# Performance work log

Hardware: AMD Instinct MI355X
Metric: run time of the kernel (lower is better)

## Reference

```python
import jax, jax.numpy as jnp
import numpy as np
import math

B, T, D = 2, 2048, 1024
H, DH = 16, 64  # n_heads, d_head
ROPE_THETA = 10000.0


def _rope_cos_sin(seq_len, d_head, dtype):
    # inv_freq over even indices, freqs[i,j] = t_i * inv_freq_j, shape [T, d_head//2]
    inv_freq = 1.0 / (ROPE_THETA ** (jnp.arange(0, d_head, 2, dtype=jnp.float32) / d_head))
    freqs = jnp.arange(seq_len, dtype=jnp.float32)[:, None] * inv_freq[None, :]
    # emb = cat(freqs, freqs); we only ever index cos[..., :d_head//2], so keep the half
    cos = jnp.cos(freqs).astype(dtype)[None, :, None, :]  # [1,T,1,DH/2]
    sin = jnp.sin(freqs).astype(dtype)[None, :, None, :]
    return cos, sin


def _apply_rotation(x, cos, sin):
    # x: [B,T,H,DH]; rotate-half style as in the torch module
    x1, x2 = x[..., : x.shape[-1] // 2], x[..., x.shape[-1] // 2 :]
    return jnp.concatenate([x1 * cos - x2 * sin, x1 * sin + x2 * cos], axis=-1)


def setup_inputs() -> dict:
    key = jax.random.key(0)
    k1, k2, k3 = jax.random.split(key, 3)
    x = jax.random.normal(k1, (B, T, D), dtype=jnp.float32)
    # torch Linear weights stored transposed here as [in, out]; init_std=0.02
    Wqkv = jax.random.normal(k2, (D, 3 * D), dtype=jnp.float32) * 0.02
    Wout = jax.random.normal(k3, (D, D), dtype=jnp.float32) * 0.02
    return {"x": x, "Wqkv": Wqkv, "Wout": Wout}


def reference(x, Wqkv, Wout):
    b, t, d = x.shape
    qkv = x @ Wqkv  # [B,T,3D]
    q, k, v = jnp.split(qkv, 3, axis=-1)
    q = q.reshape(b, t, H, DH)
    k = k.reshape(b, t, H, DH)
    v = v.reshape(b, t, H, DH)

    cos, sin = _rope_cos_sin(t, DH, x.dtype)
    q = _apply_rotation(q, cos, sin)
    k = _apply_rotation(k, cos, sin)

    scale = 1.0 / math.sqrt(DH)
    # scores: [B,H,Tq,Tk]
    scores = jnp.einsum("bqhd,bkhd->bhqk", q, k) * scale
    causal = jnp.triu(jnp.ones((t, t), dtype=bool), k=1)
    scores = jnp.where(causal[None, None, :, :], -jnp.inf, scores)
    attn = jax.nn.softmax(scores, axis=-1)
    # dropout in eval mode -> identity
    out = jnp.einsum("bhqk,bkhd->bqhd", attn, v).reshape(b, t, d)
    return out @ Wout
```

## Files before the change

kernel.cpp:

```cpp
#include <hip/hip_runtime.h>
#include <hip/hip_bf16.h>
#include <stdint.h>
#include <math.h>

#define T_SEQ 2048
#define NHEAD 16
#define NBH   32
#define BTROW 4096

typedef __bf16 bf16_t;
typedef __bf16 bf16x4_t __attribute__((ext_vector_type(4)));
typedef __bf16 bf16x8_t __attribute__((ext_vector_type(8)));
typedef float  f32x4_t  __attribute__((ext_vector_type(4)));

#define QSCALE 0.18033688011112042f

__device__ __forceinline__ f32x4_t mfma16(bf16x8_t a, bf16x8_t b, f32x4_t c) {
  return __builtin_amdgcn_mfma_f32_16x16x32_bf16(a, b, c, 0, 0, 0);
}

__device__ __forceinline__ float fast_exp2(float x) {
#if __has_builtin(__builtin_amdgcn_exp2f)
  return __builtin_amdgcn_exp2f(x);
#else
  return exp2f(x);
#endif
}

__device__ __forceinline__ void gl_lds16(const bf16_t* g, bf16_t* l) {
  __builtin_amdgcn_global_load_lds(
      (const __attribute__((address_space(1))) void*)g,
      (__attribute__((address_space(3))) void*)l, 16, 0, 0);
}

__global__ __launch_bounds__(256) void k_cast_bf16(const float* __restrict__ in,
                                                   bf16_t* __restrict__ out, int n) {
  int tid = blockIdx.x * blockDim.x + threadIdx.x;
  int stride = gridDim.x * blockDim.x;
  for (int i = tid * 4; i < n; i += stride * 4) {
    float4 a = *(const float4*)(in + i);
    bf16x4_t r = { (bf16_t)a.x, (bf16_t)a.y, (bf16_t)a.z, (bf16_t)a.w };
    *(bf16x4_t*)(out + i) = r;
  }
}

__global__ __launch_bounds__(256) void k_trans_cast(const float* __restrict__ W,
                                                    bf16_t* __restrict__ WT,
                                                    int K, int N) {
  __shared__ float tile[32][33];
  int n0 = blockIdx.x * 32, k0 = blockIdx.y * 32;
  int tx = threadIdx.x & 31, ty = threadIdx.x >> 5;
#pragma unroll
  for (int j = 0; j < 4; j++)
    tile[ty + j * 8][tx] = W[(size_t)(k0 + ty + j * 8) * N + n0 + tx];
  __syncthreads();
#pragma unroll
  for (int j = 0; j < 4; j++)
    WT[(size_t)(n0 + ty + j * 8) * K + k0 + tx] = (bf16_t)tile[tx][ty + j * 8];
}

__global__ __launch_bounds__(256) void k_rope_table(float* __restrict__ cs,
                                                    float* __restrict__ sn) {
  int i = blockIdx.x * blockDim.x + threadIdx.x;
  if (i >= T_SEQ * 32) return;
  int t = i >> 5, j = i & 31;
  float inv = powf(10000.0f, -(float)(2 * j) / 64.0f);
  float f = (float)t * inv;
  cs[i] = cosf(f);
  sn[i] = sinf(f);
}

__global__ __launch_bounds__(256) void k_gemm_qkv(const bf16_t* __restrict__ A,
                                                  const bf16_t* __restrict__ Bt,
                                                  const float* __restrict__ cs,
                                                  const float* __restrict__ sn,
                                                  bf16_t* __restrict__ Qr,
                                                  bf16_t* __restrict__ Kr,
                                                  bf16_t* __restrict__ Vt) {
  const int K = 1024;
  __shared__ __align__(16) unsigned char smem[128 * 132 * 2];
  bf16_t* As = (bf16_t*)smem;
  bf16_t* Bs = (bf16_t*)(smem + 8192);
  bf16_t* vtile = (bf16_t*)smem;

  int m0 = blockIdx.y * 128, n0 = blockIdx.x * 128;
  int tid = threadIdx.x;
  int lane = tid & 63, w = tid >> 6;
  int wr = w >> 1, wc = w & 1;
  int l15 = lane & 15, l4 = lane >> 4;

  f32x4_t acc[4][4];
#pragma unroll
  for (int m = 0; m < 4; m++)
#pragma unroll
    for (int n = 0; n < 4; n++) acc[m][n] = (f32x4_t){0.f, 0.f, 0.f, 0.f};

  for (int k0 = 0; k0 < K; k0 += 32) {
#pragma unroll
    for (int j = 0; j < 2; j++) {
      int c = j * 256 + tid;
      int row = c >> 2, kb = c & 3;
      gl_lds16(A + (size_t)(m0 + row) * K + k0 + kb * 8, As + (size_t)(j * 256 + w * 64) * 8);
      gl_lds16(Bt + (size_t)(n0 + row) * K + k0 + kb * 8, Bs + (size_t)(j * 256 + w * 64) * 8);
    }
    __syncthreads();
    bf16x8_t af[4], bfr[4];
#pragma unroll
    for (int m = 0; m < 4; m++)
      af[m] = *(const bf16x8_t*)(As + (size_t)(wr * 64 + m * 16 + l15) * 32 + l4 * 8);
#pragma unroll
    for (int n = 0; n < 4; n++)
      bfr[n] = *(const bf16x8_t*)(Bs + (size_t)(wc * 64 + n * 16 + l15) * 32 + l4 * 8);
#pragma unroll
    for (int m = 0; m < 4; m++)
#pragma unroll
      for (int n = 0; n < 4; n++) acc[m][n] = mfma16(af[m], bfr[n], acc[m][n]);
    __syncthreads();
  }

  int region = n0 >> 10;
  if (region < 2) {
    bf16_t* dst = region ? Kr : Qr;
    float qs = region ? 1.0f : QSCALE;
    int h = ((n0 & 1023) + wc * 64) >> 6;
#pragma unroll
    for (int m = 0; m < 4; m++)
#pragma unroll
      for (int r = 0; r < 4; r++) {
        int row = m0 + wr * 64 + m * 16 + l4 * 4 + r;
        int b = row >> 11, t = row & 2047;
        size_t obase = ((size_t)(b * NHEAD + h) * T_SEQ + t) * 64;
#pragma unroll
        for (int n = 0; n < 2; n++) {
          int j = n * 16 + l15;
          float c = cs[t * 32 + j], s = sn[t * 32 + j];
          float x1 = acc[m][n][r], x2 = acc[m][n + 2][r];
          dst[obase + j]      = (bf16_t)((x1 * c - x2 * s) * qs);
          dst[obase + 32 + j] = (bf16_t)((x1 * s + x2 * c) * qs);
        }
      }
  } else {
#pragma unroll
    for (int m = 0; m < 4; m++)
#pragma unroll
      for (int n = 0; n < 4; n++)
#pragma unroll
        for (int r = 0; r < 4; r++)
          vtile[(size_t)(wc * 64 + n * 16 + l15) * 132 + wr * 64 + m * 16 + l4 * 4 + r] =
              (bf16_t)acc[m][n][r];
    __syncthreads();
    int colbase = n0 - 2048;
    int b = m0 >> 11, t0l = m0 & 2047;
#pragma unroll
    for (int p = 0; p < 64; p++) {
      int idx = p * 256 + tid;
      int dl = idx >> 7, tl = idx & 127;
      int col = colbase + dl, h = col >> 6, d = col & 63;
      Vt[((size_t)(b * NHEAD + h) * 64 + d) * T_SEQ + t0l + tl] = vtile[(size_t)dl * 132 + tl];
    }
  }
}

__global__ __launch_bounds__(256) void k_gemm2(const bf16_t* __restrict__ A,
                                               const bf16_t* __restrict__ Bt,
                                               float* __restrict__ C) {
  const int N = 1024, K = 1024;
  __shared__ __align__(16) bf16_t As[64 * 32];
  __shared__ __align__(16) bf16_t Bs[128 * 32];
  int m0 = blockIdx.y * 64, n0 = blockIdx.x * 128;
  int tid = threadIdx.x;
  int lane = tid & 63, w = tid >> 6;
  int l15 = lane & 15, l4 = lane >> 4;

  f32x4_t acc[4][2];
#pragma unroll
  for (int m = 0; m < 4; m++)
#pragma unroll
    for (int n = 0; n < 2; n++) acc[m][n] = (f32x4_t){0.f, 0.f, 0.f, 0.f};

  for (int k0 = 0; k0 < K; k0 += 32) {
    {
      int row = tid >> 2, kb = tid & 3;
      gl_lds16(A + (size_t)(m0 + row) * K + k0 + kb * 8, As + (size_t)(w * 64) * 8);
    }
#pragma unroll
    for (int j = 0; j < 2; j++) {
      int c = j * 256 + tid;
      int row = c >> 2, kb = c & 3;
      gl_lds16(Bt + (size_t)(n0 + row) * K + k0 + kb * 8, Bs + (size_t)(j * 256 + w * 64) * 8);
    }
    __syncthreads();
    bf16x8_t af[4], bfr[2];
#pragma unroll
    for (int m = 0; m < 4; m++)
      af[m] = *(const bf16x8_t*)(As + (size_t)(m * 16 + l15) * 32 + l4 * 8);
#pragma unroll
    for (int n = 0; n < 2; n++)
      bfr[n] = *(const bf16x8_t*)(Bs + (size_t)(w * 32 + n * 16 + l15) * 32 + l4 * 8);
#pragma unroll
    for (int m = 0; m < 4; m++)
#pragma unroll
      for (int n = 0; n < 2; n++) acc[m][n] = mfma16(af[m], bfr[n], acc[m][n]);
    __syncthreads();
  }
#pragma unroll
  for (int m = 0; m < 4; m++)
#pragma unroll
    for (int n = 0; n < 2; n++)
#pragma unroll
      for (int r = 0; r < 4; r++) {
        int row = m0 + m * 16 + l4 * 4 + r;
        int col = n0 + w * 32 + n * 16 + l15;
        C[(size_t)row * N + col] = acc[m][n][r];
      }
}

__global__ __launch_bounds__(512, 4) void k_attn(const bf16_t* __restrict__ Qr,
                                                 const bf16_t* __restrict__ Kr,
                                                 const bf16_t* __restrict__ Vt,
                                                 bf16_t* __restrict__ Ob) {
  __shared__ __align__(16) bf16_t Ks[2][64 * 64];
  __shared__ __align__(16) bf16_t Vs[2][64 * 64];
  __shared__ __align__(16) bf16_t Ps[128 * 72];
  int flat = blockIdx.x;
  int swz = (flat & 7) * 64 + (flat >> 3);
  int pidx = swz & 15, bh = swz >> 4;
  int b = bh >> 4, h = bh & 15;
  int tid = threadIdx.x, lane = tid & 63, w = tid >> 6;
  int grp = w >> 2, wl = w & 3;
  int l15 = lane & 15, l4 = lane >> 4;

  int qb = grp ? (31 - pidx) : pidx;
  int nit = qb + 1;
  int nit_max = 32 - pidx;
  int q0 = qb * 64;

  const bf16_t* Kbh = Kr + (size_t)bh * T_SEQ * 64;
  const bf16_t* Vbh = Vt + (size_t)bh * 64 * T_SEQ;

  int srow = tid >> 3;
  int sk8 = (tid & 7) ^ (srow & 7);

  auto stage = [&](int buf, int it) {
    int kb = it * 64;
    gl_lds16(Kbh + (size_t)(kb + srow) * 64 + sk8 * 8, Ks[buf] + (size_t)(w * 64) * 8);
    gl_lds16(Vbh + (size_t)srow * T_SEQ + kb + sk8 * 8, Vs[buf] + (size_t)(w * 64) * 8);
  };

  bf16x8_t qf[2];
  size_t qbase = ((size_t)bh * T_SEQ + q0 + wl * 16 + l15) * 64;
  qf[0] = *(const bf16x8_t*)(Qr + qbase + l4 * 8);
  qf[1] = *(const bf16x8_t*)(Qr + qbase + 32 + l4 * 8);

  bf16x8_t ones;
#pragma unroll
  for (int i = 0; i < 8; i++) ones[i] = (bf16_t)1.0f;

  f32x4_t o[4];
#pragma unroll
  for (int n = 0; n < 4; n++) o[n] = (f32x4_t){0.f, 0.f, 0.f, 0.f};
  f32x4_t ls = (f32x4_t){0.f, 0.f, 0.f, 0.f};
  float m_s = -1e30f;

  stage(0, 0);

  for (int it = 0; it < nit_max; it++) {
    int cur = it & 1;
    asm volatile("s_waitcnt vmcnt(0)" ::: "memory");
    __builtin_amdgcn_s_barrier();
    if (it + 1 < nit_max) stage(cur ^ 1, it + 1);

    if (it < nit) {
      f32x4_t s[4];
      __builtin_amdgcn_s_setprio(1);
#pragma unroll
      for (int n = 0; n < 4; n++) {
        int rowK = n * 16 + l15;
        const bf16_t* kp = Ks[cur] + (size_t)rowK * 64;
        int sw = rowK & 7;
        bf16x8_t kf0 = *(const bf16x8_t*)(kp + (l4 ^ sw) * 8);
        bf16x8_t kf1 = *(const bf16x8_t*)(kp + ((l4 ^ 4) ^ sw) * 8);
        s[n] = (f32x4_t){0.f, 0.f, 0.f, 0.f};
        s[n] = mfma16(kf0, qf[0], s[n]);
        s[n] = mfma16(kf1, qf[1], s[n]);
      }
      __builtin_amdgcn_s_setprio(0);

      if (it == qb) {
#pragma unroll
        for (int n = 0; n < 4; n++)
#pragma unroll
          for (int r = 0; r < 4; r++)
            if (n * 16 + l4 * 4 + r > wl * 16 + l15) s[n][r] = -1e30f;
      }

      float t0 = fmaxf(fmaxf(s[0][0], s[0][1]), fmaxf(s[0][2], s[0][3]));
      float t1 = fmaxf(fmaxf(s[1][0], s[1][1]), fmaxf(s[1][2], s[1][3]));
      float t2 = fmaxf(fmaxf(s[2][0], s[2][1]), fmaxf(s[2][2], s[2][3]));
      float t3 = fmaxf(fmaxf(s[3][0], s[3][1]), fmaxf(s[3][2], s[3][3]));
      float mx = fmaxf(fmaxf(t0, t1), fmaxf(t2, t3));
      mx = fmaxf(mx, __shfl_xor(mx, 16, 64));
      mx = fmaxf(mx, __shfl_xor(mx, 32, 64));

      if (__any(mx - m_s > 8.0f)) {
        float mnew = fmaxf(m_s, mx);
        float alpha = fast_exp2(m_s - mnew);
        m_s = mnew;
        float ar[4];
#pragma unroll
        for (int r = 0; r < 4; r++) ar[r] = __shfl(alpha, l4 * 4 + r, 64);
#pragma unroll
        for (int n = 0; n < 4; n++)
#pragma unroll
          for (int r = 0; r < 4; r++) o[n][r] *= ar[r];
#pragma unroll
        for (int r = 0; r < 4; r++) ls[r] *= ar[r];
      }

#pragma unroll
      for (int n = 0; n < 4; n++) {
#pragma unroll
        for (int r = 0; r < 4; r++) s[n][r] = fast_exp2(s[n][r] - m_s);
        bf16x4_t pk = { (bf16_t)s[n][0], (bf16_t)s[n][1], (bf16_t)s[n][2], (bf16_t)s[n][3] };
        *(bf16x4_t*)(Ps + (size_t)(w * 16 + l15) * 72 + n * 16 + l4 * 4) = pk;
      }

      __builtin_amdgcn_s_setprio(1);
#pragma unroll
      for (int ks = 0; ks < 2; ks++) {
        bf16x8_t pa = *(const bf16x8_t*)(Ps + (size_t)(w * 16 + l15) * 72 + ks * 32 + l4 * 8);
        ls = mfma16(pa, ones, ls);
#pragma unroll
        for (int n = 0; n < 4; n++) {
          int rowV = n * 16 + l15;
          bf16x8_t vf = *(const bf16x8_t*)(Vs[cur] + (size_t)rowV * 64 +
                                           (((ks * 4 + l4) ^ (rowV & 7)) * 8));
          o[n] = mfma16(pa, vf, o[n]);
        }
      }
      __builtin_amdgcn_s_setprio(0);
    }
  }

#pragma unroll
  for (int r = 0; r < 4; r++) {
    float ir = 1.0f / ls[r];
    int q = q0 + wl * 16 + l4 * 4 + r;
    size_t off = ((size_t)(b * T_SEQ + q)) * 1024 + h * 64;
#pragma unroll
    for (int n = 0; n < 4; n++)
      Ob[off + n * 16 + l15] = (bf16_t)(o[n][r] * ir);
  }
}

extern "C" void kernel_launch(void* const* d_in, const int* in_sizes, int n_in,
                              void* d_out, int out_size, void* d_ws, size_t ws_size,
                              hipStream_t stream) {
  const float* x    = (const float*)d_in[0];
  const float* Wqkv = (const float*)d_in[1];
  const float* Wout = (const float*)d_in[2];
  float* out = (float*)d_out;
  char* ws = (char*)d_ws;

  bf16_t* wqkvT = (bf16_t*)(ws + 0);
  bf16_t* woutT = (bf16_t*)(ws + 6291456);
  bf16_t* xb    = (bf16_t*)(ws + 8388608);
  bf16_t* Qr    = (bf16_t*)(ws + 41943040);
  bf16_t* Kr    = (bf16_t*)(ws + 50331648);
  bf16_t* Vt    = (bf16_t*)(ws + 58720256);
  float*  cs    = (float*)(ws + 67108864);
  float*  sn    = (float*)(ws + 67371008);
  bf16_t* Ob    = xb;

  k_cast_bf16<<<2048, 256, 0, stream>>>(x, xb, 4096 * 1024);
  k_trans_cast<<<dim3(3072 / 32, 1024 / 32), 256, 0, stream>>>(Wqkv, wqkvT, 1024, 3072);
  k_trans_cast<<<dim3(1024 / 32, 1024 / 32), 256, 0, stream>>>(Wout, woutT, 1024, 1024);
  k_rope_table<<<(T_SEQ * 32) / 256, 256, 0, stream>>>(cs, sn);

  k_gemm_qkv<<<dim3(3072 / 128, 4096 / 128), 256, 0, stream>>>(xb, wqkvT, cs, sn, Qr, Kr, Vt);
  k_attn<<<512, 512, 0, stream>>>(Qr, Kr, Vt, Ob);
  k_gemm2<<<dim3(1024 / 128, 4096 / 64), 256, 0, stream>>>(Ob, woutT, out);
}
```

Measured before the change: 116.6 us.

## Double-buffer GEMM K-loops and split attention KV tiles across wave groups

Both GEMM kernels now double-buffer their LDS tiles so the next K-slice is prefetched while the current one runs through MFMA, with one barrier per step instead of two. The attention kernel is restructured: each block handles its paired Q tiles in two sequential passes. Within each pass the two wave groups split the KV tiles between them (even and odd), and their online-softmax partial states are merged through LDS at the end. The P scratch buffer gets an XOR swizzle. This balances causal work across waves and overlaps loads with compute, at the cost of more LDS, extra merge barriers and a pipeline restart per pass.

```diff
diff --git a/kernel.cpp b/kernel.cpp
--- a/kernel.cpp
+++ b/kernel.cpp
@@ -78,9 +78,7 @@
                                                   bf16_t* __restrict__ Kr,
                                                   bf16_t* __restrict__ Vt) {
   const int K = 1024;
-  __shared__ __align__(16) unsigned char smem[128 * 132 * 2];
-  bf16_t* As = (bf16_t*)smem;
-  bf16_t* Bs = (bf16_t*)(smem + 8192);
+  __shared__ __align__(16) unsigned char smem[33792];
   bf16_t* vtile = (bf16_t*)smem;
 
   int m0 = blockIdx.y * 128, n0 = blockIdx.x * 128;
@@ -95,7 +93,9 @@
 #pragma unroll
     for (int n = 0; n < 4; n++) acc[m][n] = (f32x4_t){0.f, 0.f, 0.f, 0.f};
 
-  for (int k0 = 0; k0 < K; k0 += 32) {
+  auto stageg = [&](int bf, int k0) {
+    bf16_t* As = (bf16_t*)(smem + bf * 16384);
+    bf16_t* Bs = (bf16_t*)(smem + 8192 + bf * 16384);
 #pragma unroll
     for (int j = 0; j < 2; j++) {
       int c = j * 256 + tid;
@@ -103,7 +103,16 @@
       gl_lds16(A + (size_t)(m0 + row) * K + k0 + kb * 8, As + (size_t)(j * 256 + w * 64) * 8);
       gl_lds16(Bt + (size_t)(n0 + row) * K + k0 + kb * 8, Bs + (size_t)(j * 256 + w * 64) * 8);
     }
-    __syncthreads();
+  };
+
+  stageg(0, 0);
+  for (int kt = 0; kt < 32; kt++) {
+    int cb = kt & 1;
+    bf16_t* As = (bf16_t*)(smem + cb * 16384);
+    bf16_t* Bs = (bf16_t*)(smem + 8192 + cb * 16384);
+    asm volatile("s_waitcnt vmcnt(0)" ::: "memory");
+    __builtin_amdgcn_s_barrier();
+    if (kt + 1 < 32) stageg(cb ^ 1, (kt + 1) * 32);
     bf16x8_t af[4], bfr[4];
 #pragma unroll
     for (int m = 0; m < 4; m++)
@@ -115,8 +124,8 @@
     for (int m = 0; m < 4; m++)
 #pragma unroll
       for (int n = 0; n < 4; n++) acc[m][n] = mfma16(af[m], bfr[n], acc[m][n]);
-    __syncthreads();
   }
+  __syncthreads();
 
   int region = n0 >> 10;
   if (region < 2) {
@@ -165,8 +174,8 @@
                                                const bf16_t* __restrict__ Bt,
                                                float* __restrict__ C) {
   const int N = 1024, K = 1024;
-  __shared__ __align__(16) bf16_t As[64 * 32];
-  __shared__ __align__(16) bf16_t Bs[128 * 32];
+  __shared__ __align__(16) bf16_t As[2][64 * 32];
+  __shared__ __align__(16) bf16_t Bs[2][128 * 32];
   int m0 = blockIdx.y * 64, n0 = blockIdx.x * 128;
   int tid = threadIdx.x;
   int lane = tid & 63, w = tid >> 6;
@@ -178,30 +187,36 @@
 #pragma unroll
     for (int n = 0; n < 2; n++) acc[m][n] = (f32x4_t){0.f, 0.f, 0.f, 0.f};
 
-  for (int k0 = 0; k0 < K; k0 += 32) {
+  auto stageg = [&](int bf, int k0) {
     {
       int row = tid >> 2, kb = tid & 3;
-      gl_lds16(A + (size_t)(m0 + row) * K + k0 + kb * 8, As + (size_t)(w * 64) * 8);
+      gl_lds16(A + (size_t)(m0 + row) * K + k0 + kb * 8, &As[bf][0] + (size_t)(w * 64) * 8);
     }
 #pragma unroll
     for (int j = 0; j < 2; j++) {
       int c = j * 256 + tid;
       int row = c >> 2, kb = c & 3;
-      gl_lds16(Bt + (size_t)(n0 + row) * K + k0 + kb * 8, Bs + (size_t)(j * 256 + w * 64) * 8);
-    }
-    __syncthreads();
+      gl_lds16(Bt + (size_t)(n0 + row) * K + k0 + kb * 8, &Bs[bf][0] + (size_t)(j * 256 + w * 64) * 8);
+    }
+  };
+
+  stageg(0, 0);
+  for (int kt = 0; kt < 32; kt++) {
+    int cb = kt & 1;
+    asm volatile("s_waitcnt vmcnt(0)" ::: "memory");
+    __builtin_amdgcn_s_barrier();
+    if (kt + 1 < 32) stageg(cb ^ 1, (kt + 1) * 32);
     bf16x8_t af[4], bfr[2];
 #pragma unroll
     for (int m = 0; m < 4; m++)
-      af[m] = *(const bf16x8_t*)(As + (size_t)(m * 16 + l15) * 32 + l4 * 8);
+      af[m] = *(const bf16x8_t*)(&As[cb][0] + (size_t)(m * 16 + l15) * 32 + l4 * 8);
 #pragma unroll
     for (int n = 0; n < 2; n++)
-      bfr[n] = *(const bf16x8_t*)(Bs + (size_t)(w * 32 + n * 16 + l15) * 32 + l4 * 8);
+      bfr[n] = *(const bf16x8_t*)(&Bs[cb][0] + (size_t)(w * 32 + n * 16 + l15) * 32 + l4 * 8);
 #pragma unroll
     for (int m = 0; m < 4; m++)
 #pragma unroll
       for (int n = 0; n < 2; n++) acc[m][n] = mfma16(af[m], bfr[n], acc[m][n]);
-    __syncthreads();
   }
 #pragma unroll
   for (int m = 0; m < 4; m++)
@@ -219,137 +234,173 @@
                                                  const bf16_t* __restrict__ Kr,
                                                  const bf16_t* __restrict__ Vt,
                                                  bf16_t* __restrict__ Ob) {
-  __shared__ __align__(16) bf16_t Ks[2][64 * 64];
-  __shared__ __align__(16) bf16_t Vs[2][64 * 64];
-  __shared__ __align__(16) bf16_t Ps[128 * 72];
+  __shared__ __align__(16) bf16_t Ks[2][2][64 * 64];
+  __shared__ __align__(16) bf16_t Vs[2][2][64 * 64];
+  __shared__ __align__(16) bf16_t Ps[8][16 * 64];
   int flat = blockIdx.x;
   int swz = (flat & 7) * 64 + (flat >> 3);
-  int pidx = swz & 15, bh = swz >> 4;
+  int pair = swz & 15, bh = swz >> 4;
   int b = bh >> 4, h = bh & 15;
   int tid = threadIdx.x, lane = tid & 63, w = tid >> 6;
   int grp = w >> 2, wl = w & 3;
   int l15 = lane & 15, l4 = lane >> 4;
 
-  int qb = grp ? (31 - pidx) : pidx;
-  int nit = qb + 1;
-  int nit_max = 32 - pidx;
-  int q0 = qb * 64;
-
   const bf16_t* Kbh = Kr + (size_t)bh * T_SEQ * 64;
   const bf16_t* Vbh = Vt + (size_t)bh * 64 * T_SEQ;
 
   int srow = tid >> 3;
   int sk8 = (tid & 7) ^ (srow & 7);
 
-  auto stage = [&](int buf, int it) {
-    int kb = it * 64;
-    gl_lds16(Kbh + (size_t)(kb + srow) * 64 + sk8 * 8, Ks[buf] + (size_t)(w * 64) * 8);
-    gl_lds16(Vbh + (size_t)srow * T_SEQ + kb + sk8 * 8, Vs[buf] + (size_t)(w * 64) * 8);
+  auto stage = [&](int buf, int i) {
+#pragma unroll
+    for (int tp = 0; tp < 2; tp++) {
+      int kb = (2 * i + tp) * 64;
+      gl_lds16(Kbh + (size_t)(kb + srow) * 64 + sk8 * 8, &Ks[buf][tp][0] + (size_t)w * 512);
+      gl_lds16(Vbh + (size_t)srow * T_SEQ + kb + sk8 * 8, &Vs[buf][tp][0] + (size_t)w * 512);
+    }
   };
 
-  bf16x8_t qf[2];
-  size_t qbase = ((size_t)bh * T_SEQ + q0 + wl * 16 + l15) * 64;
-  qf[0] = *(const bf16x8_t*)(Qr + qbase + l4 * 8);
-  qf[1] = *(const bf16x8_t*)(Qr + qbase + 32 + l4 * 8);
+  char* myPs = (char*)&Ps[w][0];
 
   bf16x8_t ones;
 #pragma unroll
   for (int i = 0; i < 8; i++) ones[i] = (bf16_t)1.0f;
 
-  f32x4_t o[4];
-#pragma unroll
-  for (int n = 0; n < 4; n++) o[n] = (f32x4_t){0.f, 0.f, 0.f, 0.f};
-  f32x4_t ls = (f32x4_t){0.f, 0.f, 0.f, 0.f};
-  float m_s = -1e30f;
-
-  stage(0, 0);
-
-  for (int it = 0; it < nit_max; it++) {
-    int cur = it & 1;
-    asm volatile("s_waitcnt vmcnt(0)" ::: "memory");
-    __builtin_amdgcn_s_barrier();
-    if (it + 1 < nit_max) stage(cur ^ 1, it + 1);
-
-    if (it < nit) {
-      f32x4_t s[4];
-      __builtin_amdgcn_s_setprio(1);
-#pragma unroll
-      for (int n = 0; n < 4; n++) {
-        int rowK = n * 16 + l15;
-        const bf16_t* kp = Ks[cur] + (size_t)rowK * 64;
-        int sw = rowK & 7;
-        bf16x8_t kf0 = *(const bf16x8_t*)(kp + (l4 ^ sw) * 8);
-        bf16x8_t kf1 = *(const bf16x8_t*)(kp + ((l4 ^ 4) ^ sw) * 8);
-        s[n] = (f32x4_t){0.f, 0.f, 0.f, 0.f};
-        s[n] = mfma16(kf0, qf[0], s[n]);
-        s[n] = mfma16(kf1, qf[1], s[n]);
+  for (int pass = 0; pass < 2; pass++) {
+    int qb = pass ? (31 - pair) : pair;
+    int q0 = qb * 64;
+    int niter = (qb + 2) >> 1;
+
+    bf16x8_t qf[2];
+    size_t qbase = ((size_t)bh * T_SEQ + q0 + wl * 16 + l15) * 64;
+    qf[0] = *(const bf16x8_t*)(Qr + qbase + l4 * 8);
+    qf[1] = *(const bf16x8_t*)(Qr + qbase + 32 + l4 * 8);
+
+    f32x4_t o[4];
+#pragma unroll
+    for (int n = 0; n < 4; n++) o[n] = (f32x4_t){0.f, 0.f, 0.f, 0.f};
+    f32x4_t ls = (f32x4_t){0.f, 0.f, 0.f, 0.f};
+    float m_s = -1e30f;
+
+    stage(0, 0);
+
+    for (int i = 0; i < niter; i++) {
+      int cur = i & 1;
+      asm volatile("s_waitcnt vmcnt(0)" ::: "memory");
+      __builtin_amdgcn_s_barrier();
+      if (i + 1 < niter) stage(cur ^ 1, i + 1);
+
+      int t = 2 * i + grp;
+      if (t <= qb) {
+        const bf16_t* Kt = &Ks[cur][grp][0];
+        const bf16_t* Vtl = &Vs[cur][grp][0];
+
+        f32x4_t s[4];
+        __builtin_amdgcn_s_setprio(1);
+#pragma unroll
+        for (int n = 0; n < 4; n++) {
+          int rowK = n * 16 + l15;
+          const bf16_t* kp = Kt + (size_t)rowK * 64;
+          int sw = rowK & 7;
+          bf16x8_t kf0 = *(const bf16x8_t*)(kp + (l4 ^ sw) * 8);
+          bf16x8_t kf1 = *(const bf16x8_t*)(kp + ((l4 ^ 4) ^ sw) * 8);
+          s[n] = (f32x4_t){0.f, 0.f, 0.f, 0.f};
+          s[n] = mfma16(kf0, qf[0], s[n]);
+          s[n] = mfma16(kf1, qf[1], s[n]);
+        }
+        __builtin_amdgcn_s_setprio(0);
+
+        if (t == qb) {
+#pragma unroll
+          for (int n = 0; n < 4; n++)
+#pragma unroll
+            for (int r = 0; r < 4; r++)
+              if (n * 16 + l4 * 4 + r > wl * 16 + l15) s[n][r] = -1e30f;
+        }
+
+        float t0 = fmaxf(fmaxf(s[0][0], s[0][1]), fmaxf(s[0][2], s[0][3]));
+        float t1 = fmaxf(fmaxf(s[1][0], s[1][1]), fmaxf(s[1][2], s[1][3]));
+        float t2 = fmaxf(fmaxf(s[2][0], s[2][1]), fmaxf(s[2][2], s[2][3]));
+        float t3 = fmaxf(fmaxf(s[3][0], s[3][1]), fmaxf(s[3][2], s[3][3]));
+        float mx = fmaxf(fmaxf(t0, t1), fmaxf(t2, t3));
+        mx = fmaxf(mx, __shfl_xor(mx, 16, 64));
+        mx = fmaxf(mx, __shfl_xor(mx, 32, 64));
+
+        if (__any(mx - m_s > 8.0f)) {
+          float mnew = fmaxf(m_s, mx);
+          float alpha = fast_exp2(m_s - mnew);
+          m_s = mnew;
+          float ar[4];
+#pragma unroll
+          for (int r = 0; r < 4; r++) ar[r] = __shfl(alpha, l4 * 4 + r, 64);
+#pragma unroll
+          for (int n = 0; n < 4; n++)
+#pragma unroll
+            for (int r = 0; r < 4; r++) o[n][r] *= ar[r];
+#pragma unroll
+          for (int r = 0; r < 4; r++) ls[r] *= ar[r];
+        }
+
+#pragma unroll
+        for (int n = 0; n < 4; n++) {
+#pragma unroll
+          for (int r = 0; r < 4; r++) s[n][r] = fast_exp2(s[n][r] - m_s);
+          bf16x4_t pk = { (bf16_t)s[n][0], (bf16_t)s[n][1], (bf16_t)s[n][2], (bf16_t)s[n][3] };
+          *(bf16x4_t*)(myPs + l15 * 128 +
+                       ((((n << 1) | (l4 >> 1)) ^ (l15 & 7)) << 4) + ((l4 & 1) << 3)) = pk;
+        }
+
+        __builtin_amdgcn_s_setprio(1);
+#pragma unroll
+        for (int ks = 0; ks < 2; ks++) {
+          bf16x8_t pa = *(const bf16x8_t*)(myPs + l15 * 128 +
+                                           ((((ks << 2) | l4) ^ (l15 & 7)) << 4));
+          ls = mfma16(pa, ones, ls);
+#pragma unroll
+          for (int n = 0; n < 4; n++) {
+            int rowV = n * 16 + l15;
+            bf16x8_t vf = *(const bf16x8_t*)(Vtl + (size_t)rowV * 64 +
+                                             (((ks * 4 + l4) ^ (rowV & 7)) * 8));
+            o[n] = mfma16(pa, vf, o[n]);
+          }
+        }
+        __builtin_amdgcn_s_setprio(0);
       }
-      __builtin_amdgcn_s_setprio(0);
-
-      if (it == qb) {
-#pragma unroll
-        for (int n = 0; n < 4; n++)
-#pragma unroll
-          for (int r = 0; r < 4; r++)
-            if (n * 16 + l4 * 4 + r > wl * 16 + l15) s[n][r] = -1e30f;
+    }
+
+    __syncthreads();
+    float* mg = (float*)&Ks[0][0][0];
+    int base = (wl * 64 + lane) * 25;
+    if (grp == 1) {
+#pragma unroll
+      for (int n = 0; n < 4; n++)
+#pragma unroll
+        for (int r = 0; r < 4; r++) mg[base + n * 4 + r] = o[n][r];
+#pragma unroll
+      for (int r = 0; r < 4; r++) mg[base + 16 + r] = ls[r];
+#pragma unroll
+      for (int r = 0; r < 4; r++) mg[base + 20 + r] = __shfl(m_s, l4 * 4 + r, 64);
+    }
+    __syncthreads();
+    if (grp == 0) {
+#pragma unroll
+      for (int r = 0; r < 4; r++) {
+        float mA = __shfl(m_s, l4 * 4 + r, 64);
+        float mB = mg[base + 20 + r];
+        float mF = fmaxf(mA, mB);
+        float fA = fast_exp2(mA - mF), fB = fast_exp2(mB - mF);
+        float lF = ls[r] * fA + mg[base + 16 + r] * fB;
+        float ir = 1.0f / lF;
+        int q = q0 + wl * 16 + l4 * 4 + r;
+        size_t off = ((size_t)(b * T_SEQ + q)) * 1024 + h * 64;
+#pragma unroll
+        for (int n = 0; n < 4; n++) {
+          float val = o[n][r] * fA + mg[base + n * 4 + r] * fB;
+          Ob[off + n * 16 + l15] = (bf16_t)(val * ir);
+        }
       }
-
-      float t0 = fmaxf(fmaxf(s[0][0], s[0][1]), fmaxf(s[0][2], s[0][3]));
-      float t1 = fmaxf(fmaxf(s[1][0], s[1][1]), fmaxf(s[1][2], s[1][3]));
-      float t2 = fmaxf(fmaxf(s[2][0], s[2][1]), fmaxf(s[2][2], s[2][3]));
-      float t3 = fmaxf(fmaxf(s[3][0], s[3][1]), fmaxf(s[3][2], s[3][3]));
-      float mx = fmaxf(fmaxf(t0, t1), fmaxf(t2, t3));
-      mx = fmaxf(mx, __shfl_xor(mx, 16, 64));
-      mx = fmaxf(mx, __shfl_xor(mx, 32, 64));
-
-      if (__any(mx - m_s > 8.0f)) {
-        float mnew = fmaxf(m_s, mx);
-        float alpha = fast_exp2(m_s - mnew);
-        m_s = mnew;
-        float ar[4];
-#pragma unroll
-        for (int r = 0; r < 4; r++) ar[r] = __shfl(alpha, l4 * 4 + r, 64);
-#pragma unroll
-        for (int n = 0; n < 4; n++)
-#pragma unroll
-          for (int r = 0; r < 4; r++) o[n][r] *= ar[r];
-#pragma unroll
-        for (int r = 0; r < 4; r++) ls[r] *= ar[r];
-      }
-
-#pragma unroll
-      for (int n = 0; n < 4; n++) {
-#pragma unroll
-        for (int r = 0; r < 4; r++) s[n][r] = fast_exp2(s[n][r] - m_s);
-        bf16x4_t pk = { (bf16_t)s[n][0], (bf16_t)s[n][1], (bf16_t)s[n][2], (bf16_t)s[n][3] };
-        *(bf16x4_t*)(Ps + (size_t)(w * 16 + l15) * 72 + n * 16 + l4 * 4) = pk;
-      }
-
-      __builtin_amdgcn_s_setprio(1);
-#pragma unroll
-      for (int ks = 0; ks < 2; ks++) {
-        bf16x8_t pa = *(const bf16x8_t*)(Ps + (size_t)(w * 16 + l15) * 72 + ks * 32 + l4 * 8);
-        ls = mfma16(pa, ones, ls);
-#pragma unroll
-        for (int n = 0; n < 4; n++) {
-          int rowV = n * 16 + l15;
-          bf16x8_t vf = *(const bf16x8_t*)(Vs[cur] + (size_t)rowV * 64 +
-                                           (((ks * 4 + l4) ^ (rowV & 7)) * 8));
-          o[n] = mfma16(pa, vf, o[n]);
-        }
-      }
-      __builtin_amdgcn_s_setprio(0);
-    }
-  }
-
-#pragma unroll
-  for (int r = 0; r < 4; r++) {
-    float ir = 1.0f / ls[r];
-    int q = q0 + wl * 16 + l4 * 4 + r;
-    size_t off = ((size_t)(b * T_SEQ + q)) * 1024 + h * 64;
-#pragma unroll
-    for (int n = 0; n < 4; n++)
-      Ob[off + n * 16 + l15] = (bf16_t)(o[n][r] * ir);
+    }
+    __syncthreads();
   }
 }
 
```

Measured after the change: 119.1 us. 2.1% more time.
